# Performance work log

Hardware: AMD Instinct MI355X
Metric: run time of the kernel (lower is better)

## Reference

```python
import jax, jax.numpy as jnp
import numpy as np

GRAPH_ALPHA = 3.0
HOP_ALPHA = 0.05
TOP_K = 30


def conv1x1(x, W, b):
    # x: [B,C,N,T], W: [O,C] -> [B,O,N,T]
    return jnp.einsum('bcnt,oc->bont', x, W) + b[None, :, None, None]


def tconv(x, W, b):
    # temporal conv along T, kernel (1,3), 'same' padding. W: [O,I,1,3]
    y = jax.lax.conv_general_dilated(x, W, (1, 1), ((0, 0), (1, 1)),
                                     dimension_numbers=('NCHW', 'OIHW', 'NCHW'))
    return y + b[None, :, None, None]


def mixprop(x, adj, W, b):
    # 1-hop mix-prop graph diffusion (gcn_depth=1, hopalpha=0.05)
    n = adj.shape[0]
    A = adj + jnp.eye(n, dtype=adj.dtype)
    A = A / A.sum(axis=1, keepdims=True)
    h = HOP_ALPHA * x + (1.0 - HOP_ALPHA) * jnp.einsum('bcvt,vw->bcwt', x, A)
    return conv1x1(jnp.concatenate([x, h], axis=1), W, b)


def st_block(x, adj, tf_w, tf_b, tg_w, tg_b, g1_w, g1_b, g2_w, g2_b,
             end_w, end_b, out_w, out_b):
    h = jnp.tanh(tconv(x, tf_w, tf_b)) * jax.nn.sigmoid(tconv(x, tg_w, tg_b))
    h = mixprop(h, adj, g1_w, g1_b) + mixprop(h, adj.T, g2_w, g2_b)
    h = jax.nn.relu(conv1x1(h, end_w, end_b))
    return conv1x1(h, out_w, out_b)


def build_adj(idx, emb1, emb2, l1_w, l1_b, l2_w, l2_b):
    e1, e2 = emb1[idx], emb2[idx]
    n1 = jnp.tanh(GRAPH_ALPHA * (e1 @ l1_w.T + l1_b))
    n2 = jnp.tanh(GRAPH_ALPHA * (e2 @ l2_w.T + l2_b))
    a = n1 @ n2.T - n2 @ n1.T
    adj = jax.nn.relu(jnp.tanh(GRAPH_ALPHA * a))
    _, top_idx = jax.lax.top_k(adj, TOP_K)
    rows = jnp.arange(adj.shape[0])[:, None]
    mask = jnp.zeros_like(adj).at[rows, top_idx].set(1.0)
    return adj * mask


def setup_inputs() -> dict:
    B, T, N, D = 16, 128, 1024, 64
    ks = jax.random.split(jax.random.key(0), 24)
    def w(i, shape):
        return jax.random.normal(ks[i], shape, dtype=jnp.float32) * 0.1
    z = lambda *s: jnp.zeros(s, jnp.float32)
    return {
        'x': jax.random.normal(ks[0], (B, T, N), dtype=jnp.float32),
        'idx': jnp.arange(N, dtype=jnp.int32),
        'emb1': w(1, (N, D)), 'emb2': w(2, (N, D)),
        'lin1_w': w(3, (D, D)), 'lin1_b': z(D),
        'lin2_w': w(4, (D, D)), 'lin2_b': z(D),
        'w_start': w(5, (16, 1)), 'b_start': z(16),
        'enc_tf_w': w(6, (16, 16, 1, 3)), 'enc_tf_b': z(16),
        'enc_tg_w': w(7, (16, 16, 1, 3)), 'enc_tg_b': z(16),
        'enc_g1_w': w(8, (16, 32)), 'enc_g1_b': z(16),
        'enc_g2_w': w(9, (16, 32)), 'enc_g2_b': z(16),
        'enc_end_w': w(10, (32, 16)), 'enc_end_b': z(32),
        'enc_out_w': w(11, (64, 32)), 'enc_out_b': z(64),
        'dec_tf_w': w(12, (64, 64, 1, 3)), 'dec_tf_b': z(64),
        'dec_tg_w': w(13, (64, 64, 1, 3)), 'dec_tg_b': z(64),
        'dec_g1_w': w(14, (64, 128)), 'dec_g1_b': z(64),
        'dec_g2_w': w(15, (64, 128)), 'dec_g2_b': z(64),
        'dec_end_w': w(16, (32, 64)), 'dec_end_b': z(32),
        'dec_out_w': w(17, (16, 32)), 'dec_out_b': z(16),
        'w_end': w(18, (1, 16)), 'b_end': z(1),
    }


def reference(x, idx, emb1, emb2, lin1_w, lin1_b, lin2_w, lin2_b,
              w_start, b_start,
              enc_tf_w, enc_tf_b, enc_tg_w, enc_tg_b, enc_g1_w, enc_g1_b,
              enc_g2_w, enc_g2_b, enc_end_w, enc_end_b, enc_out_w, enc_out_b,
              dec_tf_w, dec_tf_b, dec_tg_w, dec_tg_b, dec_g1_w, dec_g1_b,
              dec_g2_w, dec_g2_b, dec_end_w, dec_end_b, dec_out_w, dec_out_b,
              w_end, b_end):
    adj = build_adj(idx, emb1, emb2, lin1_w, lin1_b, lin2_w, lin2_b)
    h = jnp.transpose(x, (0, 2, 1))[:, None]  # [B,1,N,T]
    h = conv1x1(h, w_start, b_start)          # [B,16,N,T]
    z = st_block(h, adj, enc_tf_w, enc_tf_b, enc_tg_w, enc_tg_b,
                 enc_g1_w, enc_g1_b, enc_g2_w, enc_g2_b,
                 enc_end_w, enc_end_b, enc_out_w, enc_out_b)  # [B,64,N,T]
    y = st_block(z, adj, dec_tf_w, dec_tf_b, dec_tg_w, dec_tg_b,
                 dec_g1_w, dec_g1_b, dec_g2_w, dec_g2_b,
                 dec_end_w, dec_end_b, dec_out_w, dec_out_b)  # [B,16,N,T]
    y = conv1x1(y, w_end, b_end)               # [B,1,N,T]
    return jnp.transpose(y[:, 0], (0, 2, 1))   # [B,T,N]
```

## Files before the change

### kernel.cpp

```cpp
#include <hip/hip_runtime.h>
#include <math.h>

#define NN   1024
#define TTL  128
#define NTP  131072
#define TOPK 30

#define OEGTF_T 0
#define OEGTF_C 48
#define OEGTF_B 96
#define OEGTG_T 112
#define OEGTG_C 160
#define OEGTG_B 208
#define OEE0    224
#define OEE1    736
#define OEE2    1248
#define OEEB    1760
#define OEOUT_W 1792
#define OEOUT_B 3840
#define ODTF_B  16192
#define ODTG_B  28544
#define ODEB    34752
#define OWC     34784
#define OBC     34816
#define ODEALL  59456
#define ODTW2   65600
#define OCF     77888
#define OCG     78080
#define WTOT    78272


__global__ void k_prep_weights(
    const float* __restrict__ w_start, const float* __restrict__ b_start,
    const float* __restrict__ etf_w, const float* __restrict__ etf_b,
    const float* __restrict__ etg_w, const float* __restrict__ etg_b,
    const float* __restrict__ eg1_w, const float* __restrict__ eg1_b,
    const float* __restrict__ eg2_w, const float* __restrict__ eg2_b,
    const float* __restrict__ eend_w, const float* __restrict__ eend_b,
    const float* __restrict__ eout_w, const float* __restrict__ eout_b,
    const float* __restrict__ dtf_w, const float* __restrict__ dtf_b,
    const float* __restrict__ dtg_w, const float* __restrict__ dtg_b,
    const float* __restrict__ dg1_w, const float* __restrict__ dg1_b,
    const float* __restrict__ dg2_w, const float* __restrict__ dg2_b,
    const float* __restrict__ dend_w, const float* __restrict__ dend_b,
    const float* __restrict__ dout_w, const float* __restrict__ dout_b,
    const float* __restrict__ w_end, const float* __restrict__ b_end,
    float* __restrict__ W)
{
    int tid = blockIdx.x*blockDim.x + threadIdx.x;
    int nthr = gridDim.x*blockDim.x;
    for (int id=tid; id<96; id+=nthr){
        int which = id/48; int r = id%48; int o = r/3, k = r%3;
        const float* w = which ? etg_w : etf_w;
        double t=0.0, c=0.0;
        for (int i=0;i<16;i++){
            double wv = (double)w[(o*16+i)*3+k];
            t += wv*(double)w_start[i];
            c += wv*(double)b_start[i];
        }
        W[(which?OEGTG_T:OEGTF_T)+o*3+k] = (float)t;
        W[(which?OEGTG_C:OEGTF_C)+o*3+k] = (float)c;
    }
    for (int i=tid;i<16;i+=nthr){
        W[OEGTF_B+i] = etf_b[i];
        W[OEGTG_B+i] = etg_b[i];
    }
    for (int id=tid; id<512; id+=nthr){
        int i = id>>5, o2 = id&31;
        double s0=0.0, s1=0.0, s2=0.0;
        for (int o=0;o<16;o++){
            double m0 = (double)eg1_w[o*32+i] + (double)eg2_w[o*32+i]
                      + 0.05*((double)eg1_w[o*32+16+i] + (double)eg2_w[o*32+16+i]);
            double m1 = 0.95*(double)eg1_w[o*32+16+i];
            double m2 = 0.95*(double)eg2_w[o*32+16+i];
            double ew = (double)eend_w[o2*16+o];
            s0 += ew*m0; s1 += ew*m1; s2 += ew*m2;
        }
        W[OEE0+i*32+o2]=(float)s0; W[OEE1+i*32+o2]=(float)s1; W[OEE2+i*32+o2]=(float)s2;
    }
    for (int o2=tid; o2<32; o2+=nthr){
        double s = (double)eend_b[o2];
        for (int o=0;o<16;o++) s += (double)eend_w[o2*16+o]*((double)eg1_b[o]+(double)eg2_b[o]);
        W[OEEB+o2] = (float)s;
    }
    for (int i=tid;i<64;i+=nthr){
        W[ODTF_B+i]=dtf_b[i]; W[ODTG_B+i]=dtg_b[i];
    }
    for (int id=tid; id<12288; id+=nthr){
        int oc = id/3072; int rem = id%3072; int j = rem/96; int q = rem%96;
        const float* w = (q<48) ? dtf_w : dtg_w;
        int q2 = (q<48) ? q : q-48;
        int o = q2/3, k = q2%3;
        double s = 0.0;
        for (int i=0;i<64;i++)
            s += (double)w[((oc*16+o)*64+i)*3+k]*(double)eout_w[i*32+j];
        W[ODTW2+id] = (float)s;
    }
    for (int id=tid; id<384; id+=nthr){
        int which = id/192; int r = id%192;
        int oc = r/48; int q = r%48; int o = q/3, k = q%3;
        const float* w = which ? dtg_w : dtf_w;
        double s = 0.0;
        for (int i=0;i<64;i++)
            s += (double)w[((oc*16+o)*64+i)*3+k]*(double)eout_b[i];
        W[(which?OCG:OCF) + oc*48 + o*3 + k] = (float)s;
    }
    for (int id=tid; id<6144; id+=nthr){
        int i = id/96, j = id%96;
        double s = 0.0;
        if (j < 32){
            int o2 = j;
            for (int o=0;o<64;o++){
                double m1 = 0.95*(double)dg1_w[o*128+64+i];
                s += (double)dend_w[o2*64+o]*m1;
            }
        } else if (j < 64){
            int o2 = j-32;
            for (int o=0;o<64;o++){
                double m2 = 0.95*(double)dg2_w[o*128+64+i];
                s += (double)dend_w[o2*64+o]*m2;
            }
        } else {
            int o2 = j-64;
            for (int o=0;o<64;o++){
                double m0 = (double)dg1_w[o*128+i] + (double)dg2_w[o*128+i]
                          + 0.05*((double)dg1_w[o*128+64+i] + (double)dg2_w[o*128+64+i]);
                s += (double)dend_w[o2*64+o]*m0;
            }
        }
        W[ODEALL+id] = (float)s;
    }
    for (int o2=tid; o2<32; o2+=nthr){
        double s = (double)dend_b[o2];
        for (int o=0;o<64;o++) s += (double)dend_w[o2*64+o]*((double)dg1_b[o]+(double)dg2_b[o]);
        W[ODEB+o2] = (float)s;
        double wc = 0.0;
        for (int o3=0;o3<16;o3++) wc += (double)w_end[o3]*(double)dout_w[o3*32+o2];
        W[OWC+o2] = (float)wc;
    }
    if (tid==0){
        double bc = (double)b_end[0];
        for (int o3=0;o3<16;o3++) bc += (double)w_end[o3]*(double)dout_b[o3];
        W[OBC] = (float)bc;
    }
}

__global__ void k_emb(const int* __restrict__ idxp,
                      const float* __restrict__ emb1, const float* __restrict__ emb2,
                      const float* __restrict__ l1w, const float* __restrict__ l1b,
                      const float* __restrict__ l2w, const float* __restrict__ l2b,
                      double* __restrict__ n1, double* __restrict__ n2)
{
    int id = blockIdx.x*blockDim.x + threadIdx.x;
    int i = id>>6, d = id&63;
    int ii = idxp[i];
    double a1 = (double)l1b[d], a2 = (double)l2b[d];
    for (int k=0;k<64;k++){
        a1 += (double)emb1[ii*64+k]*(double)l1w[d*64+k];
        a2 += (double)emb2[ii*64+k]*(double)l2w[d*64+k];
    }
    n1[id] = tanh(3.0*a1);
    n2[id] = tanh(3.0*a2);
}

__global__ __launch_bounds__(64) void k_topk(
    const double* __restrict__ n1, const double* __restrict__ n2,
    int* __restrict__ topc, double* __restrict__ topv,
    double* __restrict__ rs1, double* __restrict__ colsum)
{
    __shared__ double arow[NN];
    __shared__ double sn1[64], sn2[64];
    int i = blockIdx.x, lane = threadIdx.x;
    sn1[lane] = n1[i*64+lane];
    sn2[lane] = n2[i*64+lane];
    __syncthreads();
    for (int jb=0;jb<16;jb++){
        int j = jb*64 + lane;
        const double* p2 = n2 + (long)j*64;
        const double* p1 = n1 + (long)j*64;
        double d1v=0.0, d2v=0.0;
        for (int d=0;d<64;d++){ d1v += sn1[d]*p2[d]; d2v += sn2[d]*p1[d]; }
        double a = tanh(3.0*(d1v - d2v));
        arow[j] = a>0.0 ? a : 0.0;
    }
    __syncthreads();
    double lv = -2.0; int lj = 1<<30;
    for (int jb=0;jb<16;jb++){
        int j = jb*64+lane;
        double v = arow[j];
        if (v>lv || (v==lv && j<lj)){ lv=v; lj=j; }
    }
    double rsum = 0.0;
    for (int r=0;r<TOPK;r++){
        double bv = lv; int bj = lj;
        for (int off=32; off>=1; off>>=1){
            double ov = __shfl_xor(bv, off, 64);
            int    oj = __shfl_xor(bj, off, 64);
            if (ov>bv || (ov==bv && oj<bj)){ bv=ov; bj=oj; }
        }
        if (lane == (bj & 63)){
            arow[bj] = -2.0;
            lv = -2.0; lj = 1<<30;
            for (int jb=0;jb<16;jb++){
                int j = jb*64+lane;
                double v = arow[j];
                if (v>lv || (v==lv && j<lj)){ lv=v; lj=j; }
            }
        }
        if (lane == 0){
            topc[i*TOPK+r] = bj;
            topv[i*TOPK+r] = bv;
            if (bv > 0.0) atomicAdd(&colsum[bj], bv);
        }
        rsum += (bv > 0.0 ? bv : 0.0);
    }
    if (lane == 0) rs1[i] = 1.0 + rsum;
}

__global__ void k_csc(const int* __restrict__ topc, const double* __restrict__ topv,
                      const double* __restrict__ rs1,
                      int* __restrict__ ccount, int* __restrict__ cidx, float* __restrict__ cw)
{
    int w = blockIdx.x*blockDim.x + threadIdx.x;
    if (w >= NN) return;
    double rv = rs1[w];
    for (int r=0;r<TOPK;r++){
        double v = topv[w*TOPK+r];
        if (v > 0.0){
            int col = topc[w*TOPK+r];
            int pos = atomicAdd(&ccount[col], 1);
            cidx[(long)col*NN+pos] = w;
            cw  [(long)col*NN+pos] = (float)(v / rv);
        }
    }
}

__global__ void k_pad(int* __restrict__ ccount, int* __restrict__ cidx, float* __restrict__ cw)
{
    int col = blockIdx.x*blockDim.x + threadIdx.x;
    if (col >= NN) return;
    int cnt = ccount[col];
    int padded = (cnt + 7) & ~7;
    for (int e = cnt; e < padded; e++){
        cidx[(long)col*NN + e] = 0;
        cw  [(long)col*NN + e] = 0.0f;
    }
    ccount[col] = padded;
}

__global__ void k_post1(const double* __restrict__ colsum, const double* __restrict__ rs1,
                        double* __restrict__ rs2, float* __restrict__ d1, float* __restrict__ d2)
{
    int v = blockIdx.x*blockDim.x + threadIdx.x;
    if (v >= NN) return;
    double r2 = 1.0 + colsum[v];
    rs2[v] = r2;
    d2[v] = (float)(1.0/r2);
    d1[v] = (float)(1.0/rs1[v]);
}

__global__ void k_post2(const int* __restrict__ topc, const double* __restrict__ topv,
                        const double* __restrict__ rs2,
                        int* __restrict__ topc2, float* __restrict__ ew2b)
{
    int e = blockIdx.x*blockDim.x + threadIdx.x;
    if (e >= NN*32) return;
    int w = e>>5, r = e&31;
    if (r < TOPK){
        double v = topv[w*TOPK+r];
        int c = topc[w*TOPK+r];
        topc2[e] = (v > 0.0) ? c : 0;
        ew2b[e]  = (v > 0.0) ? (float)(v / rs2[c]) : 0.0f;
    } else {
        topc2[e] = 0;
        ew2b[e]  = 0.0f;
    }
}


__global__ __launch_bounds__(256) void k_enc_gg(const float* __restrict__ x,
    float* __restrict__ eg, float* __restrict__ es1, float* __restrict__ es2,
    const float* __restrict__ Wt,
    const int* __restrict__ ccount, const int* __restrict__ cidx, const float* __restrict__ cw,
    const int* __restrict__ topc2, const float* __restrict__ ew2b,
    const float* __restrict__ d1, const float* __restrict__ d2,
    long S, int b0)
{
    __shared__ float4 lds4[NN];
    int tid = threadIdx.x, c = blockIdx.y, cb = blockIdx.z, t0 = blockIdx.x*4;
    float ft[3], fc[3], gt[3], gcc[3];
    #pragma unroll
    for (int k=0;k<3;k++){
        ft[k]=Wt[OEGTF_T+c*3+k]; fc[k]=Wt[OEGTF_C+c*3+k];
        gt[k]=Wt[OEGTG_T+c*3+k]; gcc[k]=Wt[OEGTG_C+c*3+k];
    }
    float fb = Wt[OEGTF_B+c], gb = Wt[OEGTG_B+c];
    const float* xb = x + (long)(b0+cb)*NTP + (long)t0*NN;
    long base = (long)c*S + (long)cb*NTP + (long)t0*NN;
    bool hl0 = (t0>0), hr3 = (t0+4<TTL);
    for (int q=0;q<4;q++){
        int v = q*256 + tid;
        float xm = hl0 ? xb[v-NN] : 0.0f;
        float x0 = xb[v], x1 = xb[v+NN], x2 = xb[v+2*NN], x3 = xb[v+3*NN];
        float xq = hr3 ? xb[v+4*NN] : 0.0f;
        float g0,g1,g2,g3;
        {
            float atf = fb + ft[1]*x0 + fc[1], atg = gb + gt[1]*x0 + gcc[1];
            if (hl0){ atf += ft[0]*xm + fc[0]; atg += gt[0]*xm + gcc[0]; }
            atf += ft[2]*x1 + fc[2]; atg += gt[2]*x1 + gcc[2];
            g0 = tanhf(atf)/(1.0f+expf(-atg));
        }
        {
            float atf = fb + ft[0]*x0 + fc[0] + ft[1]*x1 + fc[1] + ft[2]*x2 + fc[2];
            float atg = gb + gt[0]*x0 + gcc[0] + gt[1]*x1 + gcc[1] + gt[2]*x2 + gcc[2];
            g1 = tanhf(atf)/(1.0f+expf(-atg));
        }
        {
            float atf = fb + ft[0]*x1 + fc[0] + ft[1]*x2 + fc[1] + ft[2]*x3 + fc[2];
            float atg = gb + gt[0]*x1 + gcc[0] + gt[1]*x2 + gcc[1] + gt[2]*x3 + gcc[2];
            g2 = tanhf(atf)/(1.0f+expf(-atg));
        }
        {
            float atf = fb + ft[0]*x2 + fc[0] + ft[1]*x3 + fc[1];
            float atg = gb + gt[0]*x2 + gcc[0] + gt[1]*x3 + gcc[1];
            if (hr3){ atf += ft[2]*xq + fc[2]; atg += gt[2]*xq + gcc[2]; }
            g3 = tanhf(atf)/(1.0f+expf(-atg));
        }
        lds4[v] = make_float4(g0,g1,g2,g3);
        eg[base+v] = g0; eg[base+NN+v] = g1; eg[base+2*NN+v] = g2; eg[base+3*NN+v] = g3;
    }
    __syncthreads();
    for (int wb=0;wb<4;wb++){
        int w = wb*256 + tid;
        float4 gw = lds4[w];
        float dv = d1[w];
        float a0=gw.x*dv, a1=gw.y*dv, a2=gw.z*dv, a3=gw.w*dv;
        int cnt = ccount[w];
        const int4*   ci4 = (const int4*)  (cidx + (long)w*NN);
        const float4* cw4 = (const float4*)(cw   + (long)w*NN);
        for (int e=0; e<cnt; e+=8){
            int4 ia = ci4[e>>2], ib = ci4[(e>>2)+1];
            float4 wa = cw4[e>>2], wc = cw4[(e>>2)+1];
            float4 s;
            s = lds4[ia.x]; a0 += wa.x*s.x; a1 += wa.x*s.y; a2 += wa.x*s.z; a3 += wa.x*s.w;
            s = lds4[ia.y]; a0 += wa.y*s.x; a1 += wa.y*s.y; a2 += wa.y*s.z; a3 += wa.y*s.w;
            s = lds4[ia.z]; a0 += wa.z*s.x; a1 += wa.z*s.y; a2 += wa.z*s.z; a3 += wa.z*s.w;
            s = lds4[ia.w]; a0 += wa.w*s.x; a1 += wa.w*s.y; a2 += wa.w*s.z; a3 += wa.w*s.w;
            s = lds4[ib.x]; a0 += wc.x*s.x; a1 += wc.x*s.y; a2 += wc.x*s.z; a3 += wc.x*s.w;
            s = lds4[ib.y]; a0 += wc.y*s.x; a1 += wc.y*s.y; a2 += wc.y*s.z; a3 += wc.y*s.w;
            s = lds4[ib.z]; a0 += wc.z*s.x; a1 += wc.z*s.y; a2 += wc.z*s.z; a3 += wc.z*s.w;
            s = lds4[ib.w]; a0 += wc.w*s.x; a1 += wc.w*s.y; a2 += wc.w*s.z; a3 += wc.w*s.w;
        }
        es1[base+w]=a0; es1[base+NN+w]=a1; es1[base+2*NN+w]=a2; es1[base+3*NN+w]=a3;
        float dw = d2[w];
        float b0a=gw.x*dw, b1a=gw.y*dw, b2a=gw.z*dw, b3a=gw.w*dw;
        const int4*   tc4 = (const int4*)  (topc2 + w*32);
        const float4* e24 = (const float4*)(ew2b  + w*32);
        #pragma unroll
        for (int r=0;r<8;r++){
            int4 ic = tc4[r]; float4 wv = e24[r];
            float4 s;
            s = lds4[ic.x]; b0a += wv.x*s.x; b1a += wv.x*s.y; b2a += wv.x*s.z; b3a += wv.x*s.w;
            s = lds4[ic.y]; b0a += wv.y*s.x; b1a += wv.y*s.y; b2a += wv.y*s.z; b3a += wv.y*s.w;
            s = lds4[ic.z]; b0a += wv.z*s.x; b1a += wv.z*s.y; b2a += wv.z*s.z; b3a += wv.z*s.w;
            s = lds4[ic.w]; b0a += wv.w*s.x; b1a += wv.w*s.y; b2a += wv.w*s.z; b3a += wv.w*s.w;
        }
        es2[base+w]=b0a; es2[base+NN+w]=b1a; es2[base+2*NN+w]=b2a; es2[base+3*NN+w]=b3a;
    }
}

__global__ __launch_bounds__(256) void k_enc_tail(const float* __restrict__ Bp,
    float* __restrict__ E32, const float* __restrict__ Wt, long S)
{
    long p = (long)blockIdx.x*256 + threadIdx.x;
    float e[32];
    #pragma unroll
    for (int o2=0;o2<32;o2++) e[o2] = Wt[OEEB+o2];
    for (int i=0;i<16;i++){
        float a = Bp[(long)i*S+p], b = Bp[(long)(16+i)*S+p], c = Bp[(long)(32+i)*S+p];
        const float* w0 = Wt+OEE0+i*32;
        const float* w1 = Wt+OEE1+i*32;
        const float* w2 = Wt+OEE2+i*32;
        #pragma unroll
        for (int o2=0;o2<32;o2++) e[o2] += w0[o2]*a + w1[o2]*b + w2[o2]*c;
    }
    #pragma unroll
    for (int o2=0;o2<32;o2++){
        float v = e[o2];
        E32[(long)o2*S+p] = v>0.0f ? v : 0.0f;
    }
}

__global__ __launch_bounds__(256) void k_dec_gate(const float* __restrict__ E32,
    float* __restrict__ g, const float* __restrict__ Wt, long S)
{
    int oc = blockIdx.y;
    long pos = (long)blockIdx.x*256 + threadIdx.x;
    int t = (int)((pos>>10) & (TTL-1));
    bool hasL = (t>0), hasR = (t<TTL-1);
    float af[16], ag[16];
    #pragma unroll
    for (int o=0;o<16;o++){
        float bf = Wt[ODTF_B+oc*16+o] + Wt[OCF+oc*48+o*3+1];
        float bg = Wt[ODTG_B+oc*16+o] + Wt[OCG+oc*48+o*3+1];
        if (hasL){ bf += Wt[OCF+oc*48+o*3];   bg += Wt[OCG+oc*48+o*3]; }
        if (hasR){ bf += Wt[OCF+oc*48+o*3+2]; bg += Wt[OCG+oc*48+o*3+2]; }
        af[o]=bf; ag[o]=bg;
    }
    #pragma unroll 1
    for (int j=0;j<32;j++){
        const float* xp = E32 + (long)j*S + pos;
        float xc = xp[0];
        float xl = hasL ? xp[-NN] : 0.0f;
        float xr = hasR ? xp[NN]  : 0.0f;
        const float* wfg = Wt + ODTW2 + (long)(oc*32+j)*96;
        #pragma unroll
        for (int o=0;o<16;o++){
            af[o] += wfg[o*3]*xl + wfg[o*3+1]*xc + wfg[o*3+2]*xr;
            ag[o] += wfg[48+o*3]*xl + wfg[48+o*3+1]*xc + wfg[48+o*3+2]*xr;
        }
    }
    #pragma unroll
    for (int o=0;o<16;o++){
        g[(long)(oc*16+o)*S + pos] = tanhf(af[o])/(1.0f+expf(-ag[o]));
    }
}

__global__ __launch_bounds__(256) void k_dec_conv(const float* __restrict__ g,
    float* __restrict__ P12, float* __restrict__ P0p,
    const float* __restrict__ Wt, long S)
{
    long p = (long)blockIdx.x*256 + threadIdx.x;
    float a0[32], a1[32], a2[32];
    #pragma unroll
    for (int jj=0;jj<32;jj++){ a1[jj]=0.0f; a2[jj]=0.0f; a0[jj]=Wt[ODEB+jj]; }
    #pragma unroll 1
    for (int i=0;i<64;i++){
        float gv = g[(long)i*S+p];
        const float* wr = Wt + ODEALL + i*96;
        #pragma unroll
        for (int jj=0;jj<32;jj++){
            a1[jj] += wr[jj]*gv;
            a2[jj] += wr[32+jj]*gv;
            a0[jj] += wr[64+jj]*gv;
        }
    }
    #pragma unroll
    for (int jj=0;jj<32;jj++){
        P12[(long)jj*S+p]      = a1[jj];
        P12[(long)(32+jj)*S+p] = a2[jj];
        P0p[(long)jj*S+p]      = a0[jj];
    }
}

__global__ __launch_bounds__(256) void k_graph32f(const float* __restrict__ P1,
    const float* __restrict__ P2, const float* __restrict__ P0,
    float* __restrict__ part,
    const int* __restrict__ ccount, const int* __restrict__ cidx, const float* __restrict__ cw,
    const int* __restrict__ topc2, const float* __restrict__ ew2b,
    const float* __restrict__ d1, const float* __restrict__ d2,
    const float* __restrict__ Wt, long S)
{
    __shared__ float4 lds4[NN];
    int tid = threadIdx.x;
    int grp = blockIdx.y, cb = blockIdx.z, t0 = blockIdx.x*4;
    long tbase = (long)cb*NTP + (long)t0*NN;
    float res[4][4];
    #pragma unroll
    for (int wb=0;wb<4;wb++){
        #pragma unroll
        for (int k=0;k<4;k++) res[wb][k]=0.0f;
    }
    float q1[4][4];
    for (int c4=0;c4<4;c4++){
        int ch = grp*4 + c4;
        long base = (long)ch*S + tbase;
        if (c4) __syncthreads();
        const float* s1 = P1 + base;
        for (int q=0;q<4;q++){
            int v = q*256 + tid;
            lds4[v] = make_float4(s1[v], s1[v+NN], s1[v+2*NN], s1[v+3*NN]);
        }
        __syncthreads();
        for (int wb=0;wb<4;wb++){
            int w = wb*256 + tid;
            float4 gv = lds4[w];
            float dv = d1[w];
            float a0=gv.x*dv, a1=gv.y*dv, a2=gv.z*dv, a3=gv.w*dv;
            int cnt = ccount[w];
            const int4*   ci4 = (const int4*)  (cidx + (long)w*NN);
            const float4* cw4 = (const float4*)(cw   + (long)w*NN);
            for (int e=0; e<cnt; e+=8){
                int4 ia = ci4[e>>2], ib = ci4[(e>>2)+1];
                float4 wa = cw4[e>>2], wc2 = cw4[(e>>2)+1];
                float4 s;
                s = lds4[ia.x]; a0 += wa.x*s.x; a1 += wa.x*s.y; a2 += wa.x*s.z; a3 += wa.x*s.w;
                s = lds4[ia.y]; a0 += wa.y*s.x; a1 += wa.y*s.y; a2 += wa.y*s.z; a3 += wa.y*s.w;
                s = lds4[ia.z]; a0 += wa.z*s.x; a1 += wa.z*s.y; a2 += wa.z*s.z; a3 += wa.z*s.w;
                s = lds4[ia.w]; a0 += wa.w*s.x; a1 += wa.w*s.y; a2 += wa.w*s.z; a3 += wa.w*s.w;
                s = lds4[ib.x]; a0 += wc2.x*s.x; a1 += wc2.x*s.y; a2 += wc2.x*s.z; a3 += wc2.x*s.w;
                s = lds4[ib.y]; a0 += wc2.y*s.x; a1 += wc2.y*s.y; a2 += wc2.y*s.z; a3 += wc2.y*s.w;
                s = lds4[ib.z]; a0 += wc2.z*s.x; a1 += wc2.z*s.y; a2 += wc2.z*s.z; a3 += wc2.z*s.w;
                s = lds4[ib.w]; a0 += wc2.w*s.x; a1 += wc2.w*s.y; a2 += wc2.w*s.z; a3 += wc2.w*s.w;
            }
            q1[wb][0]=a0; q1[wb][1]=a1; q1[wb][2]=a2; q1[wb][3]=a3;
        }
        __syncthreads();
        const float* s2 = P2 + base;
        for (int q=0;q<4;q++){
            int v = q*256 + tid;
            lds4[v] = make_float4(s2[v], s2[v+NN], s2[v+2*NN], s2[v+3*NN]);
        }
        __syncthreads();
        float wc = Wt[OWC+ch];
        const float* p0 = P0 + base;
        for (int wb=0;wb<4;wb++){
            int w = wb*256 + tid;
            float4 gv = lds4[w];
            float dw = d2[w];
            float c0=gv.x*dw, c1=gv.y*dw, c2=gv.z*dw, c3=gv.w*dw;
            const int4*   tc4 = (const int4*)  (topc2 + w*32);
            const float4* e24 = (const float4*)(ew2b  + w*32);
            #pragma unroll
            for (int r=0;r<8;r++){
                int4 ic = tc4[r]; float4 wv = e24[r];
                float4 s;
                s = lds4[ic.x]; c0 += wv.x*s.x; c1 += wv.x*s.y; c2 += wv.x*s.z; c3 += wv.x*s.w;
                s = lds4[ic.y]; c0 += wv.y*s.x; c1 += wv.y*s.y; c2 += wv.y*s.z; c3 += wv.y*s.w;
                s = lds4[ic.z]; c0 += wv.z*s.x; c1 += wv.z*s.y; c2 += wv.z*s.z; c3 += wv.z*s.w;
                s = lds4[ic.w]; c0 += wv.w*s.x; c1 += wv.w*s.y; c2 += wv.w*s.z; c3 += wv.w*s.w;
            }
            float e0 = p0[w]        + q1[wb][0] + c0;
            float e1 = p0[NN+w]     + q1[wb][1] + c1;
            float e2 = p0[2*NN+w]   + q1[wb][2] + c2;
            float e3 = p0[3*NN+w]   + q1[wb][3] + c3;
            e0 = e0>0.0f?e0:0.0f; e1 = e1>0.0f?e1:0.0f;
            e2 = e2>0.0f?e2:0.0f; e3 = e3>0.0f?e3:0.0f;
            res[wb][0] += wc*e0; res[wb][1] += wc*e1;
            res[wb][2] += wc*e2; res[wb][3] += wc*e3;
        }
    }
    long pb = (long)grp*S + tbase;
    for (int wb=0;wb<4;wb++){
        int w = wb*256 + tid;
        part[pb+w]      = res[wb][0];
        part[pb+NN+w]   = res[wb][1];
        part[pb+2*NN+w] = res[wb][2];
        part[pb+3*NN+w] = res[wb][3];
    }
}

__global__ __launch_bounds__(256) void k_comb(const float* __restrict__ part,
    const float* __restrict__ Wt, float* __restrict__ out, long S, int b0)
{
    long p = (long)blockIdx.x*256 + threadIdx.x;
    float r = Wt[OBC];
    #pragma unroll
    for (int gp=0; gp<8; gp++) r += part[(long)gp*S+p];
    out[(long)b0*NTP + p] = r;
}


extern "C" void kernel_launch(void* const* d_in, const int* in_sizes, int n_in,
                              void* d_out, int out_size, void* d_ws, size_t ws_size,
                              hipStream_t stream)
{
    const float* x      = (const float*)d_in[0];
    const int*   idx    = (const int*)  d_in[1];
    const float* emb1   = (const float*)d_in[2];
    const float* emb2   = (const float*)d_in[3];
    const float* lin1_w = (const float*)d_in[4];
    const float* lin1_b = (const float*)d_in[5];
    const float* lin2_w = (const float*)d_in[6];
    const float* lin2_b = (const float*)d_in[7];
    const float* w_start= (const float*)d_in[8];
    const float* b_start= (const float*)d_in[9];
    const float* etf_w  = (const float*)d_in[10];
    const float* etf_b  = (const float*)d_in[11];
    const float* etg_w  = (const float*)d_in[12];
    const float* etg_b  = (const float*)d_in[13];
    const float* eg1_w  = (const float*)d_in[14];
    const float* eg1_b  = (const float*)d_in[15];
    const float* eg2_w  = (const float*)d_in[16];
    const float* eg2_b  = (const float*)d_in[17];
    const float* eend_w = (const float*)d_in[18];
    const float* eend_b = (const float*)d_in[19];
    const float* eout_w = (const float*)d_in[20];
    const float* eout_b = (const float*)d_in[21];
    const float* dtf_w  = (const float*)d_in[22];
    const float* dtf_b  = (const float*)d_in[23];
    const float* dtg_w  = (const float*)d_in[24];
    const float* dtg_b  = (const float*)d_in[25];
    const float* dg1_w  = (const float*)d_in[26];
    const float* dg1_b  = (const float*)d_in[27];
    const float* dg2_w  = (const float*)d_in[28];
    const float* dg2_b  = (const float*)d_in[29];
    const float* dend_w = (const float*)d_in[30];
    const float* dend_b = (const float*)d_in[31];
    const float* dout_w = (const float*)d_in[32];
    const float* dout_b = (const float*)d_in[33];
    const float* w_end  = (const float*)d_in[34];
    const float* b_end  = (const float*)d_in[35];
    float* out = (float*)d_out;

    char* basep = (char*)d_ws;
    size_t cur = 0;
    auto alloc = [&](size_t bytes)->void* {
        void* p = basep + cur;
        cur = (cur + bytes + 511) & ~(size_t)511;
        return p;
    };
    float*  W     = (float*) alloc(WTOT*sizeof(float));
    double* n1    = (double*)alloc(65536*sizeof(double));
    double* n2    = (double*)alloc(65536*sizeof(double));
    double* topv  = (double*)alloc((size_t)NN*TOPK*sizeof(double));
    int*    topc  = (int*)   alloc((size_t)NN*TOPK*sizeof(int));
    double* rs1   = (double*)alloc(NN*sizeof(double));
    double* rs2   = (double*)alloc(NN*sizeof(double));
    double* colsum= (double*)alloc(NN*sizeof(double));
    float*  d1a   = (float*) alloc(NN*sizeof(float));
    float*  d2a   = (float*) alloc(NN*sizeof(float));
    int*    topc2 = (int*)   alloc((size_t)NN*32*sizeof(int));
    float*  ew2b  = (float*) alloc((size_t)NN*32*sizeof(float));
    int*    ccount= (int*)   alloc(NN*sizeof(int));
    int*    cidx  = (int*)   alloc((size_t)NN*NN*sizeof(int));
    float*  cw    = (float*) alloc((size_t)NN*NN*sizeof(float));

    size_t perb = (size_t)176 * NTP * sizeof(float);
    int CB = 1;
    for (int c = 16; c >= 1; c >>= 1){
        if (cur + perb*(size_t)c <= ws_size){ CB = c; break; }
    }
    long S = (long)CB * NTP;
    float* A = (float*)alloc((size_t)64*S*sizeof(float));
    float* B = (float*)alloc((size_t)48*S*sizeof(float));
    float* C = (float*)alloc((size_t)64*S*sizeof(float));

    (void)hipMemsetAsync(colsum, 0, NN*sizeof(double), stream);
    (void)hipMemsetAsync(ccount, 0, NN*sizeof(int), stream);

    k_prep_weights<<<32,256,0,stream>>>(
        w_start,b_start, etf_w,etf_b, etg_w,etg_b, eg1_w,eg1_b, eg2_w,eg2_b,
        eend_w,eend_b, eout_w,eout_b, dtf_w,dtf_b, dtg_w,dtg_b, dg1_w,dg1_b,
        dg2_w,dg2_b, dend_w,dend_b, dout_w,dout_b, w_end,b_end, W);
    k_emb<<<256,256,0,stream>>>(idx, emb1, emb2, lin1_w, lin1_b, lin2_w, lin2_b, n1, n2);
    k_topk<<<NN,64,0,stream>>>(n1, n2, topc, topv, rs1, colsum);
    k_csc<<<4,256,0,stream>>>(topc, topv, rs1, ccount, cidx, cw);
    k_pad<<<4,256,0,stream>>>(ccount, cidx, cw);
    k_post1<<<4,256,0,stream>>>(colsum, rs1, rs2, d1a, d2a);
    k_post2<<<(NN*32+255)/256,256,0,stream>>>(topc, topv, rs2, topc2, ew2b);

    int nch = 16 / CB;
    for (int ch=0; ch<nch; ch++){
        int b0 = ch*CB;
        k_enc_gg<<<dim3(32,16,CB),256,0,stream>>>(x, B, B+(long)16*S, B+(long)32*S, W,
            ccount,cidx,cw, topc2,ew2b, d1a,d2a, S, b0);
        k_enc_tail<<<512*CB,256,0,stream>>>(B, A, W, S);
        k_dec_gate<<<dim3(512*CB,4),256,0,stream>>>(A, C, W, S);
        k_dec_conv<<<512*CB,256,0,stream>>>(C, A, B, W, S);
        k_graph32f<<<dim3(32,8,CB),256,0,stream>>>(A, A+(long)32*S, B, C,
            ccount,cidx,cw, topc2,ew2b, d1a,d2a, W, S);
        k_comb<<<512*CB,256,0,stream>>>(C, W, out, S, b0);
    }
    (void)in_sizes; (void)n_in; (void)out_size;
}
```

Before: 3.952 ms.

## Process eight timesteps per graph block and split decoder conv across two blocks

The sparse graph-propagation kernels (encoder and decoder) now handle 8 timesteps per block instead of 4, using two float4 LDS arrays. Each gathered sparse index and weight then feeds twice as many accumulations, which amortizes index and weight loads and LDS gather overhead. The decoder 1x1 conv is split across a second grid dimension so one block computes P1/P2 and another computes P0, cutting per-thread register arrays from 96 to 64 or 32 and raising parallelism. The cost is more registers and LDS per graph block, half as many graph blocks, and the decoder input g being read twice.

```diff
diff --git a/kernel.cpp b/kernel.cpp
--- a/kernel.cpp
+++ b/kernel.cpp
@@ -286,8 +286,9 @@
     const float* __restrict__ d1, const float* __restrict__ d2,
     long S, int b0)
 {
-    __shared__ float4 lds4[NN];
-    int tid = threadIdx.x, c = blockIdx.y, cb = blockIdx.z, t0 = blockIdx.x*4;
+    __shared__ float4 lA[NN];
+    __shared__ float4 lB[NN];
+    int tid = threadIdx.x, c = blockIdx.y, cb = blockIdx.z, t0 = blockIdx.x*8;
     float ft[3], fc[3], gt[3], gcc[3];
     #pragma unroll
     for (int k=0;k<3;k++){
@@ -297,75 +298,82 @@
     float fb = Wt[OEGTF_B+c], gb = Wt[OEGTG_B+c];
     const float* xb = x + (long)(b0+cb)*NTP + (long)t0*NN;
     long base = (long)c*S + (long)cb*NTP + (long)t0*NN;
-    bool hl0 = (t0>0), hr3 = (t0+4<TTL);
+    bool hl0 = (t0>0), hr7 = (t0+8<TTL);
     for (int q=0;q<4;q++){
         int v = q*256 + tid;
-        float xm = hl0 ? xb[v-NN] : 0.0f;
-        float x0 = xb[v], x1 = xb[v+NN], x2 = xb[v+2*NN], x3 = xb[v+3*NN];
-        float xq = hr3 ? xb[v+4*NN] : 0.0f;
-        float g0,g1,g2,g3;
-        {
-            float atf = fb + ft[1]*x0 + fc[1], atg = gb + gt[1]*x0 + gcc[1];
-            if (hl0){ atf += ft[0]*xm + fc[0]; atg += gt[0]*xm + gcc[0]; }
-            atf += ft[2]*x1 + fc[2]; atg += gt[2]*x1 + gcc[2];
-            g0 = tanhf(atf)/(1.0f+expf(-atg));
-        }
-        {
-            float atf = fb + ft[0]*x0 + fc[0] + ft[1]*x1 + fc[1] + ft[2]*x2 + fc[2];
-            float atg = gb + gt[0]*x0 + gcc[0] + gt[1]*x1 + gcc[1] + gt[2]*x2 + gcc[2];
-            g1 = tanhf(atf)/(1.0f+expf(-atg));
-        }
-        {
-            float atf = fb + ft[0]*x1 + fc[0] + ft[1]*x2 + fc[1] + ft[2]*x3 + fc[2];
-            float atg = gb + gt[0]*x1 + gcc[0] + gt[1]*x2 + gcc[1] + gt[2]*x3 + gcc[2];
-            g2 = tanhf(atf)/(1.0f+expf(-atg));
-        }
-        {
-            float atf = fb + ft[0]*x2 + fc[0] + ft[1]*x3 + fc[1];
-            float atg = gb + gt[0]*x2 + gcc[0] + gt[1]*x3 + gcc[1];
-            if (hr3){ atf += ft[2]*xq + fc[2]; atg += gt[2]*xq + gcc[2]; }
-            g3 = tanhf(atf)/(1.0f+expf(-atg));
-        }
-        lds4[v] = make_float4(g0,g1,g2,g3);
-        eg[base+v] = g0; eg[base+NN+v] = g1; eg[base+2*NN+v] = g2; eg[base+3*NN+v] = g3;
+        float xr[10];
+        xr[0] = hl0 ? xb[v-NN] : 0.0f;
+        #pragma unroll
+        for (int k=0;k<8;k++) xr[k+1] = xb[v+(long)k*NN];
+        xr[9] = hr7 ? xb[v+(long)8*NN] : 0.0f;
+        float gg[8];
+        #pragma unroll
+        for (int k=0;k<8;k++){
+            float atf = fb + ft[1]*xr[k+1] + fc[1];
+            float atg = gb + gt[1]*xr[k+1] + gcc[1];
+            bool hL = (k>0) || hl0;
+            bool hR = (k<7) || hr7;
+            if (hL){ atf += ft[0]*xr[k] + fc[0]; atg += gt[0]*xr[k] + gcc[0]; }
+            if (hR){ atf += ft[2]*xr[k+2] + fc[2]; atg += gt[2]*xr[k+2] + gcc[2]; }
+            gg[k] = tanhf(atf)/(1.0f+expf(-atg));
+            eg[base + (long)k*NN + v] = gg[k];
+        }
+        lA[v] = make_float4(gg[0],gg[1],gg[2],gg[3]);
+        lB[v] = make_float4(gg[4],gg[5],gg[6],gg[7]);
     }
     __syncthreads();
     for (int wb=0;wb<4;wb++){
         int w = wb*256 + tid;
-        float4 gw = lds4[w];
+        float4 ga = lA[w], gbv = lB[w];
         float dv = d1[w];
-        float a0=gw.x*dv, a1=gw.y*dv, a2=gw.z*dv, a3=gw.w*dv;
+        float a0=ga.x*dv, a1=ga.y*dv, a2=ga.z*dv, a3=ga.w*dv;
+        float a4=gbv.x*dv, a5=gbv.y*dv, a6=gbv.z*dv, a7=gbv.w*dv;
         int cnt = ccount[w];
         const int4*   ci4 = (const int4*)  (cidx + (long)w*NN);
         const float4* cw4 = (const float4*)(cw   + (long)w*NN);
-        for (int e=0; e<cnt; e+=8){
-            int4 ia = ci4[e>>2], ib = ci4[(e>>2)+1];
-            float4 wa = cw4[e>>2], wc = cw4[(e>>2)+1];
-            float4 s;
-            s = lds4[ia.x]; a0 += wa.x*s.x; a1 += wa.x*s.y; a2 += wa.x*s.z; a3 += wa.x*s.w;
-            s = lds4[ia.y]; a0 += wa.y*s.x; a1 += wa.y*s.y; a2 += wa.y*s.z; a3 += wa.y*s.w;
-            s = lds4[ia.z]; a0 += wa.z*s.x; a1 += wa.z*s.y; a2 += wa.z*s.z; a3 += wa.z*s.w;
-            s = lds4[ia.w]; a0 += wa.w*s.x; a1 += wa.w*s.y; a2 += wa.w*s.z; a3 += wa.w*s.w;
-            s = lds4[ib.x]; a0 += wc.x*s.x; a1 += wc.x*s.y; a2 += wc.x*s.z; a3 += wc.x*s.w;
-            s = lds4[ib.y]; a0 += wc.y*s.x; a1 += wc.y*s.y; a2 += wc.y*s.z; a3 += wc.y*s.w;
-            s = lds4[ib.z]; a0 += wc.z*s.x; a1 += wc.z*s.y; a2 += wc.z*s.z; a3 += wc.z*s.w;
-            s = lds4[ib.w]; a0 += wc.w*s.x; a1 += wc.w*s.y; a2 += wc.w*s.z; a3 += wc.w*s.w;
+        for (int e=0; e<cnt; e+=4){
+            int4 ia = ci4[e>>2];
+            float4 wa = cw4[e>>2];
+            float4 s, u;
+            s = lA[ia.x]; u = lB[ia.x];
+            a0 += wa.x*s.x; a1 += wa.x*s.y; a2 += wa.x*s.z; a3 += wa.x*s.w;
+            a4 += wa.x*u.x; a5 += wa.x*u.y; a6 += wa.x*u.z; a7 += wa.x*u.w;
+            s = lA[ia.y]; u = lB[ia.y];
+            a0 += wa.y*s.x; a1 += wa.y*s.y; a2 += wa.y*s.z; a3 += wa.y*s.w;
+            a4 += wa.y*u.x; a5 += wa.y*u.y; a6 += wa.y*u.z; a7 += wa.y*u.w;
+            s = lA[ia.z]; u = lB[ia.z];
+            a0 += wa.z*s.x; a1 += wa.z*s.y; a2 += wa.z*s.z; a3 += wa.z*s.w;
+            a4 += wa.z*u.x; a5 += wa.z*u.y; a6 += wa.z*u.z; a7 += wa.z*u.w;
+            s = lA[ia.w]; u = lB[ia.w];
+            a0 += wa.w*s.x; a1 += wa.w*s.y; a2 += wa.w*s.z; a3 += wa.w*s.w;
+            a4 += wa.w*u.x; a5 += wa.w*u.y; a6 += wa.w*u.z; a7 += wa.w*u.w;
         }
         es1[base+w]=a0; es1[base+NN+w]=a1; es1[base+2*NN+w]=a2; es1[base+3*NN+w]=a3;
+        es1[base+4*NN+w]=a4; es1[base+5*NN+w]=a5; es1[base+6*NN+w]=a6; es1[base+7*NN+w]=a7;
         float dw = d2[w];
-        float b0a=gw.x*dw, b1a=gw.y*dw, b2a=gw.z*dw, b3a=gw.w*dw;
+        a0=ga.x*dw; a1=ga.y*dw; a2=ga.z*dw; a3=ga.w*dw;
+        a4=gbv.x*dw; a5=gbv.y*dw; a6=gbv.z*dw; a7=gbv.w*dw;
         const int4*   tc4 = (const int4*)  (topc2 + w*32);
         const float4* e24 = (const float4*)(ew2b  + w*32);
         #pragma unroll
         for (int r=0;r<8;r++){
             int4 ic = tc4[r]; float4 wv = e24[r];
-            float4 s;
-            s = lds4[ic.x]; b0a += wv.x*s.x; b1a += wv.x*s.y; b2a += wv.x*s.z; b3a += wv.x*s.w;
-            s = lds4[ic.y]; b0a += wv.y*s.x; b1a += wv.y*s.y; b2a += wv.y*s.z; b3a += wv.y*s.w;
-            s = lds4[ic.z]; b0a += wv.z*s.x; b1a += wv.z*s.y; b2a += wv.z*s.z; b3a += wv.z*s.w;
-            s = lds4[ic.w]; b0a += wv.w*s.x; b1a += wv.w*s.y; b2a += wv.w*s.z; b3a += wv.w*s.w;
-        }
-        es2[base+w]=b0a; es2[base+NN+w]=b1a; es2[base+2*NN+w]=b2a; es2[base+3*NN+w]=b3a;
+            float4 s, u;
+            s = lA[ic.x]; u = lB[ic.x];
+            a0 += wv.x*s.x; a1 += wv.x*s.y; a2 += wv.x*s.z; a3 += wv.x*s.w;
+            a4 += wv.x*u.x; a5 += wv.x*u.y; a6 += wv.x*u.z; a7 += wv.x*u.w;
+            s = lA[ic.y]; u = lB[ic.y];
+            a0 += wv.y*s.x; a1 += wv.y*s.y; a2 += wv.y*s.z; a3 += wv.y*s.w;
+            a4 += wv.y*u.x; a5 += wv.y*u.y; a6 += wv.y*u.z; a7 += wv.y*u.w;
+            s = lA[ic.z]; u = lB[ic.z];
+            a0 += wv.z*s.x; a1 += wv.z*s.y; a2 += wv.z*s.z; a3 += wv.z*s.w;
+            a4 += wv.z*u.x; a5 += wv.z*u.y; a6 += wv.z*u.z; a7 += wv.z*u.w;
+            s = lA[ic.w]; u = lB[ic.w];
+            a0 += wv.w*s.x; a1 += wv.w*s.y; a2 += wv.w*s.z; a3 += wv.w*s.w;
+            a4 += wv.w*u.x; a5 += wv.w*u.y; a6 += wv.w*u.z; a7 += wv.w*u.w;
+        }
+        es2[base+w]=a0; es2[base+NN+w]=a1; es2[base+2*NN+w]=a2; es2[base+3*NN+w]=a3;
+        es2[base+4*NN+w]=a4; es2[base+5*NN+w]=a5; es2[base+6*NN+w]=a6; es2[base+7*NN+w]=a7;
     }
 }
 
@@ -427,29 +435,40 @@
 }
 
 __global__ __launch_bounds__(256) void k_dec_conv(const float* __restrict__ g,
-    float* __restrict__ P12, float* __restrict__ P0p,
+    float* __restrict__ Cp, float* __restrict__ P0p,
     const float* __restrict__ Wt, long S)
 {
     long p = (long)blockIdx.x*256 + threadIdx.x;
-    float a0[32], a1[32], a2[32];
-    #pragma unroll
-    for (int jj=0;jj<32;jj++){ a1[jj]=0.0f; a2[jj]=0.0f; a0[jj]=Wt[ODEB+jj]; }
-    #pragma unroll 1
-    for (int i=0;i<64;i++){
-        float gv = g[(long)i*S+p];
-        const float* wr = Wt + ODEALL + i*96;
+    int jc = blockIdx.y;
+    if (jc == 0){
+        float a1[32], a2[32];
+        #pragma unroll
+        for (int jj=0;jj<32;jj++){ a1[jj]=0.0f; a2[jj]=0.0f; }
+        #pragma unroll 1
+        for (int i=0;i<64;i++){
+            float gv = g[(long)i*S+p];
+            const float* wr = Wt + ODEALL + i*96;
+            #pragma unroll
+            for (int jj=0;jj<32;jj++){ a1[jj] += wr[jj]*gv; a2[jj] += wr[32+jj]*gv; }
+        }
         #pragma unroll
         for (int jj=0;jj<32;jj++){
-            a1[jj] += wr[jj]*gv;
-            a2[jj] += wr[32+jj]*gv;
-            a0[jj] += wr[64+jj]*gv;
-        }
-    }
-    #pragma unroll
-    for (int jj=0;jj<32;jj++){
-        P12[(long)jj*S+p]      = a1[jj];
-        P12[(long)(32+jj)*S+p] = a2[jj];
-        P0p[(long)jj*S+p]      = a0[jj];
+            Cp[(long)jj*S+p] = a1[jj];
+            Cp[(long)(32+jj)*S+p] = a2[jj];
+        }
+    } else {
+        float a0[32];
+        #pragma unroll
+        for (int jj=0;jj<32;jj++) a0[jj] = Wt[ODEB+jj];
+        #pragma unroll 1
+        for (int i=0;i<64;i++){
+            float gv = g[(long)i*S+p];
+            const float* wr = Wt + ODEALL + i*96 + 64;
+            #pragma unroll
+            for (int jj=0;jj<32;jj++) a0[jj] += wr[jj]*gv;
+        }
+        #pragma unroll
+        for (int jj=0;jj<32;jj++) P0p[(long)jj*S+p] = a0[jj];
     }
 }
 
@@ -461,17 +480,18 @@
     const float* __restrict__ d1, const float* __restrict__ d2,
     const float* __restrict__ Wt, long S)
 {
-    __shared__ float4 lds4[NN];
+    __shared__ float4 lA[NN];
+    __shared__ float4 lB[NN];
     int tid = threadIdx.x;
-    int grp = blockIdx.y, cb = blockIdx.z, t0 = blockIdx.x*4;
+    int grp = blockIdx.y, cb = blockIdx.z, t0 = blockIdx.x*8;
     long tbase = (long)cb*NTP + (long)t0*NN;
-    float res[4][4];
+    float res[4][8];
     #pragma unroll
     for (int wb=0;wb<4;wb++){
         #pragma unroll
-        for (int k=0;k<4;k++) res[wb][k]=0.0f;
-    }
-    float q1[4][4];
+        for (int k=0;k<8;k++) res[wb][k]=0.0f;
+    }
+    float q1[4][8];
     for (int c4=0;c4<4;c4++){
         int ch = grp*4 + c4;
         long base = (long)ch*S + tbase;
@@ -479,74 +499,98 @@
         const float* s1 = P1 + base;
         for (int q=0;q<4;q++){
             int v = q*256 + tid;
-            lds4[v] = make_float4(s1[v], s1[v+NN], s1[v+2*NN], s1[v+3*NN]);
+            lA[v] = make_float4(s1[v], s1[v+NN], s1[v+2*NN], s1[v+3*NN]);
+            lB[v] = make_float4(s1[v+4*NN], s1[v+5*NN], s1[v+6*NN], s1[v+7*NN]);
         }
         __syncthreads();
         for (int wb=0;wb<4;wb++){
             int w = wb*256 + tid;
-            float4 gv = lds4[w];
+            float4 ga = lA[w], gbv = lB[w];
             float dv = d1[w];
-            float a0=gv.x*dv, a1=gv.y*dv, a2=gv.z*dv, a3=gv.w*dv;
+            float a0=ga.x*dv, a1=ga.y*dv, a2=ga.z*dv, a3=ga.w*dv;
+            float a4=gbv.x*dv, a5=gbv.y*dv, a6=gbv.z*dv, a7=gbv.w*dv;
             int cnt = ccount[w];
             const int4*   ci4 = (const int4*)  (cidx + (long)w*NN);
             const float4* cw4 = (const float4*)(cw   + (long)w*NN);
-            for (int e=0; e<cnt; e+=8){
-                int4 ia = ci4[e>>2], ib = ci4[(e>>2)+1];
-                float4 wa = cw4[e>>2], wc2 = cw4[(e>>2)+1];
-                float4 s;
-                s = lds4[ia.x]; a0 += wa.x*s.x; a1 += wa.x*s.y; a2 += wa.x*s.z; a3 += wa.x*s.w;
-                s = lds4[ia.y]; a0 += wa.y*s.x; a1 += wa.y*s.y; a2 += wa.y*s.z; a3 += wa.y*s.w;
-                s = lds4[ia.z]; a0 += wa.z*s.x; a1 += wa.z*s.y; a2 += wa.z*s.z; a3 += wa.z*s.w;
-                s = lds4[ia.w]; a0 += wa.w*s.x; a1 += wa.w*s.y; a2 += wa.w*s.z; a3 += wa.w*s.w;
-                s = lds4[ib.x]; a0 += wc2.x*s.x; a1 += wc2.x*s.y; a2 += wc2.x*s.z; a3 += wc2.x*s.w;
-                s = lds4[ib.y]; a0 += wc2.y*s.x; a1 += wc2.y*s.y; a2 += wc2.y*s.z; a3 += wc2.y*s.w;
-                s = lds4[ib.z]; a0 += wc2.z*s.x; a1 += wc2.z*s.y; a2 += wc2.z*s.z; a3 += wc2.z*s.w;
-                s = lds4[ib.w]; a0 += wc2.w*s.x; a1 += wc2.w*s.y; a2 += wc2.w*s.z; a3 += wc2.w*s.w;
+            for (int e=0; e<cnt; e+=4){
+                int4 ia = ci4[e>>2];
+                float4 wa = cw4[e>>2];
+                float4 s, u;
+                s = lA[ia.x]; u = lB[ia.x];
+                a0 += wa.x*s.x; a1 += wa.x*s.y; a2 += wa.x*s.z; a3 += wa.x*s.w;
+                a4 += wa.x*u.x; a5 += wa.x*u.y; a6 += wa.x*u.z; a7 += wa.x*u.w;
+                s = lA[ia.y]; u = lB[ia.y];
+                a0 += wa.y*s.x; a1 += wa.y*s.y; a2 += wa.y*s.z; a3 += wa.y*s.w;
+                a4 += wa.y*u.x; a5 += wa.y*u.y; a6 += wa.y*u.z; a7 += wa.y*u.w;
+                s = lA[ia.z]; u = lB[ia.z];
+                a0 += wa.z*s.x; a1 += wa.z*s.y; a2 += wa.z*s.z; a3 += wa.z*s.w;
+                a4 += wa.z*u.x; a5 += wa.z*u.y; a6 += wa.z*u.z; a7 += wa.z*u.w;
+                s = lA[ia.w]; u = lB[ia.w];
+                a0 += wa.w*s.x; a1 += wa.w*s.y; a2 += wa.w*s.z; a3 += wa.w*s.w;
+                a4 += wa.w*u.x; a5 += wa.w*u.y; a6 += wa.w*u.z; a7 += wa.w*u.w;
             }
             q1[wb][0]=a0; q1[wb][1]=a1; q1[wb][2]=a2; q1[wb][3]=a3;
+            q1[wb][4]=a4; q1[wb][5]=a5; q1[wb][6]=a6; q1[wb][7]=a7;
         }
         __syncthreads();
         const float* s2 = P2 + base;
         for (int q=0;q<4;q++){
             int v = q*256 + tid;
-            lds4[v] = make_float4(s2[v], s2[v+NN], s2[v+2*NN], s2[v+3*NN]);
+            lA[v] = make_float4(s2[v], s2[v+NN], s2[v+2*NN], s2[v+3*NN]);
+            lB[v] = make_float4(s2[v+4*NN], s2[v+5*NN], s2[v+6*NN], s2[v+7*NN]);
         }
         __syncthreads();
         float wc = Wt[OWC+ch];
         const float* p0 = P0 + base;
         for (int wb=0;wb<4;wb++){
             int w = wb*256 + tid;
-            float4 gv = lds4[w];
+            float4 ga = lA[w], gbv = lB[w];
             float dw = d2[w];
-            float c0=gv.x*dw, c1=gv.y*dw, c2=gv.z*dw, c3=gv.w*dw;
+            float a0=ga.x*dw, a1=ga.y*dw, a2=ga.z*dw, a3=ga.w*dw;
+            float a4=gbv.x*dw, a5=gbv.y*dw, a6=gbv.z*dw, a7=gbv.w*dw;
             const int4*   tc4 = (const int4*)  (topc2 + w*32);
             const float4* e24 = (const float4*)(ew2b  + w*32);
             #pragma unroll
             for (int r=0;r<8;r++){
                 int4 ic = tc4[r]; float4 wv = e24[r];
-                float4 s;
-                s = lds4[ic.x]; c0 += wv.x*s.x; c1 += wv.x*s.y; c2 += wv.x*s.z; c3 += wv.x*s.w;
-                s = lds4[ic.y]; c0 += wv.y*s.x; c1 += wv.y*s.y; c2 += wv.y*s.z; c3 += wv.y*s.w;
-                s = lds4[ic.z]; c0 += wv.z*s.x; c1 += wv.z*s.y; c2 += wv.z*s.z; c3 += wv.z*s.w;
-                s = lds4[ic.w]; c0 += wv.w*s.x; c1 += wv.w*s.y; c2 += wv.w*s.z; c3 += wv.w*s.w;
+                float4 s, u;
+                s = lA[ic.x]; u = lB[ic.x];
+                a0 += wv.x*s.x; a1 += wv.x*s.y; a2 += wv.x*s.z; a3 += wv.x*s.w;
+                a4 += wv.x*u.x; a5 += wv.x*u.y; a6 += wv.x*u.z; a7 += wv.x*u.w;
+                s = lA[ic.y]; u = lB[ic.y];
+                a0 += wv.y*s.x; a1 += wv.y*s.y; a2 += wv.y*s.z; a3 += wv.y*s.w;
+                a4 += wv.y*u.x; a5 += wv.y*u.y; a6 += wv.y*u.z; a7 += wv.y*u.w;
+                s = lA[ic.z]; u = lB[ic.z];
+                a0 += wv.z*s.x; a1 += wv.z*s.y; a2 += wv.z*s.z; a3 += wv.z*s.w;
+                a4 += wv.z*u.x; a5 += wv.z*u.y; a6 += wv.z*u.z; a7 += wv.z*u.w;
+                s = lA[ic.w]; u = lB[ic.w];
+                a0 += wv.w*s.x; a1 += wv.w*s.y; a2 += wv.w*s.z; a3 += wv.w*s.w;
+                a4 += wv.w*u.x; a5 += wv.w*u.y; a6 += wv.w*u.z; a7 += wv.w*u.w;
             }
-            float e0 = p0[w]        + q1[wb][0] + c0;
-            float e1 = p0[NN+w]     + q1[wb][1] + c1;
-            float e2 = p0[2*NN+w]   + q1[wb][2] + c2;
-            float e3 = p0[3*NN+w]   + q1[wb][3] + c3;
+            float e0,e1,e2,e3,e4,e5,e6,e7;
+            e0 = p0[w]      + q1[wb][0] + a0;
+            e1 = p0[NN+w]   + q1[wb][1] + a1;
+            e2 = p0[2*NN+w] + q1[wb][2] + a2;
+            e3 = p0[3*NN+w] + q1[wb][3] + a3;
+            e4 = p0[4*NN+w] + q1[wb][4] + a4;
+            e5 = p0[5*NN+w] + q1[wb][5] + a5;
+            e6 = p0[6*NN+w] + q1[wb][6] + a6;
+            e7 = p0[7*NN+w] + q1[wb][7] + a7;
             e0 = e0>0.0f?e0:0.0f; e1 = e1>0.0f?e1:0.0f;
             e2 = e2>0.0f?e2:0.0f; e3 = e3>0.0f?e3:0.0f;
+            e4 = e4>0.0f?e4:0.0f; e5 = e5>0.0f?e5:0.0f;
+            e6 = e6>0.0f?e6:0.0f; e7 = e7>0.0f?e7:0.0f;
             res[wb][0] += wc*e0; res[wb][1] += wc*e1;
             res[wb][2] += wc*e2; res[wb][3] += wc*e3;
+            res[wb][4] += wc*e4; res[wb][5] += wc*e5;
+            res[wb][6] += wc*e6; res[wb][7] += wc*e7;
         }
     }
     long pb = (long)grp*S + tbase;
     for (int wb=0;wb<4;wb++){
         int w = wb*256 + tid;
-        part[pb+w]      = res[wb][0];
-        part[pb+NN+w]   = res[wb][1];
-        part[pb+2*NN+w] = res[wb][2];
-        part[pb+3*NN+w] = res[wb][3];
+        #pragma unroll
+        for (int k=0;k<8;k++) part[pb+(long)k*NN+w] = res[wb][k];
     }
 }
 
@@ -653,12 +697,12 @@
     int nch = 16 / CB;
     for (int ch=0; ch<nch; ch++){
         int b0 = ch*CB;
-        k_enc_gg<<<dim3(32,16,CB),256,0,stream>>>(x, B, B+(long)16*S, B+(long)32*S, W,
+        k_enc_gg<<<dim3(16,16,CB),256,0,stream>>>(x, B, B+(long)16*S, B+(long)32*S, W,
             ccount,cidx,cw, topc2,ew2b, d1a,d2a, S, b0);
         k_enc_tail<<<512*CB,256,0,stream>>>(B, A, W, S);
         k_dec_gate<<<dim3(512*CB,4),256,0,stream>>>(A, C, W, S);
-        k_dec_conv<<<512*CB,256,0,stream>>>(C, A, B, W, S);
-        k_graph32f<<<dim3(32,8,CB),256,0,stream>>>(A, A+(long)32*S, B, C,
+        k_dec_conv<<<dim3(512*CB,2),256,0,stream>>>(C, A, B, W, S);
+        k_graph32f<<<dim3(16,8,CB),256,0,stream>>>(A, A+(long)32*S, B, C,
             ccount,cidx,cw, topc2,ew2b, d1a,d2a, W, S);
         k_comb<<<512*CB,256,0,stream>>>(C, W, out, S, b0);
     }
```

Measured after the change: 3.625 ms. -8.3%, faster.
